# Kernel tuning notes

Measured on AMD Instinct MI355X. Metric: run time of the kernel, lower is better.

Reference implementation:

```python
import jax, jax.numpy as jnp
import numpy as np

EPS = 1e-5  # PyTorch BatchNorm2d default eps


def _batchnorm(x, gamma, beta):
    # training-mode BN over (N, T, V) per channel; x: [N, C, T, V]
    mean = jnp.mean(x, axis=(0, 2, 3), keepdims=True)
    var = jnp.var(x, axis=(0, 2, 3), keepdims=True)
    inv = jax.lax.rsqrt(var + EPS)
    return (x - mean) * inv * gamma[None, :, None, None] + beta[None, :, None, None]


def setup_inputs() -> dict:
    key = jax.random.key(0)
    ks = jax.random.split(key, 8)
    N, Cin, Cout, T, V, S = 64, 64, 128, 300, 25, 3
    x = jax.random.normal(ks[0], (N, Cin, T, V), dtype=jnp.float32)
    A = jax.random.uniform(ks[1], (S, V, V), dtype=jnp.float32)
    # per-subset 1x1 conv weights/biases (kaiming-ish scale)
    W = jax.random.normal(ks[2], (S, Cout, Cin), dtype=jnp.float32) / np.sqrt(Cin)
    b = jax.random.normal(ks[3], (S, Cout), dtype=jnp.float32) * 0.01
    alpha = jnp.zeros((1,), dtype=jnp.float32)
    bn_gamma = jnp.ones((Cout,), dtype=jnp.float32)
    bn_beta = jnp.zeros((Cout,), dtype=jnp.float32)
    # residual down path (in_channels != out_channels): conv1x1 + BN
    down_W = jax.random.normal(ks[4], (Cout, Cin), dtype=jnp.float32) / np.sqrt(Cin)
    down_b = jax.random.normal(ks[5], (Cout,), dtype=jnp.float32) * 0.01
    down_gamma = jnp.ones((Cout,), dtype=jnp.float32)
    down_beta = jnp.zeros((Cout,), dtype=jnp.float32)
    return {
        "x": x, "A": A, "W": W, "b": b, "alpha": alpha,
        "bn_gamma": bn_gamma, "bn_beta": bn_beta,
        "down_W": down_W, "down_b": down_b,
        "down_gamma": down_gamma, "down_beta": down_beta,
    }


def reference(x, A, W, b, alpha, bn_gamma, bn_beta, down_W, down_b, down_gamma, down_beta):
    V = x.shape[-1]
    eye = jnp.eye(V, dtype=x.dtype)
    A_adj = A + alpha[0] * eye[None]  # [S, V, V]
    # sum_s conv1x1_s( x @ A_s ): fuse adjacency matmul, 1x1 conv, subset sum
    y_agg = jnp.einsum('nctv,svw,soc->notw', x, A_adj, W)
    y_agg = y_agg + jnp.sum(b, axis=0)[None, :, None, None]
    y = _batchnorm(y_agg, bn_gamma, bn_beta)
    # residual down: 1x1 conv + BN (in_channels != out_channels)
    res = jnp.einsum('nctv,oc->notv', x, down_W) + down_b[None, :, None, None]
    res = _batchnorm(res, down_gamma, down_beta)
    return jax.nn.relu(y + res)
```

## Files before the change

kernel.cpp:

```cpp
#include <hip/hip_runtime.h>
#include <hip/hip_bf16.h>

#define N_   64
#define CIN  64
#define COUT 128
#define T_   300
#define V_   25
#define S_   3
#define NTV  (N_ * T_ * V_)

#define TS     10
#define NTB    (T_ / TS)
#define NBLK   (N_ * NTB)
#define RED_ROWS   64
#define RED_BLOCKS (NBLK / RED_ROWS)

#define WS_P    0
#define WS_P2   (WS_P + NBLK * 512)
#define WS_COEF (WS_P2 + RED_BLOCKS * 512)
#define WS_WF   (WS_COEF + 512)
#define WS_WSF  (WS_WF + 16384)
#define WS_AF   (WS_WSF + 16384)

typedef __attribute__((ext_vector_type(8))) short short8;
typedef __attribute__((ext_vector_type(4))) float f32x4;

#define LDS_BARRIER() asm volatile("s_waitcnt lgkmcnt(0)\n\ts_barrier" ::: "memory")

__device__ __forceinline__ unsigned short bfbits(float f) {
    union { __hip_bfloat16 h; unsigned short u; } cv;
    cv.h = __float2bfloat16(f);
    return cv.u;
}
__device__ __forceinline__ unsigned int pack2(float lo, float hi) {
    return (unsigned int)bfbits(lo) | ((unsigned int)bfbits(hi) << 16);
}

__device__ __forceinline__ int zoff(int nl, int k) {
    int slot = (k >> 3) ^ (nl & 31);
    return nl * 512 + slot * 16 + (k & 7) * 2;
}

__global__ __launch_bounds__(256) void k_prep(const float* __restrict__ W,
                                              const float* __restrict__ dW,
                                              const float* __restrict__ A,
                                              const float* __restrict__ alpha,
                                              unsigned short* __restrict__ Wf,
                                              unsigned short* __restrict__ Af) {
    int i = blockIdx.x * 256 + threadIdx.x;
    {
        int j = i & 7, lane = (i >> 3) & 63, ks = (i >> 9) & 7;
        int oh2 = i >> 12;
        int o = oh2 * 16 + (lane & 15);
        int k = ks * 32 + (lane >> 4) * 8 + j;
        float wv = (k < 192) ? W[(k >> 6) * (COUT * CIN) + o * CIN + (k & 63)]
                             : dW[o * CIN + (k - 192)];
        Wf[i] = bfbits(wv);
    }
    if (i < 4096) {
        int j = i & 7, lane = (i >> 3) & 63, wf = (i >> 9) & 1, s = i >> 10;
        int v = (lane >> 4) * 8 + j, w = wf * 16 + (lane & 15);
        float av;
        if (s < 3)
            av = (v < V_ && w < V_)
                   ? A[(s * V_ + v) * V_ + w] + ((v == w) ? alpha[0] : 0.f)
                   : 0.f;
        else
            av = (v == w && v < V_) ? 1.f : 0.f;
        Af[i] = bfbits(av);
    }
}

__global__ __launch_bounds__(256) void k_prep2(const float* __restrict__ W,
                                               const float* __restrict__ dW,
                                               const float* __restrict__ coef,
                                               unsigned short* __restrict__ Wsf) {
    int i = blockIdx.x * 256 + threadIdx.x;
    int j = i & 7, lane = (i >> 3) & 63, ks = (i >> 9) & 7;
    int oh2 = i >> 12;
    int o = oh2 * 16 + (lane & 15);
    int k = ks * 32 + (lane >> 4) * 8 + j;
    float wv = (k < 192) ? W[(k >> 6) * (COUT * CIN) + o * CIN + (k & 63)]
                         : dW[o * CIN + (k - 192)];
    float sc = (k < 192) ? coef[o] : coef[COUT + o];
    Wsf[i] = bfbits(wv * sc);
}

struct XRaw { f32x4 a0, a1; float s; };

__device__ __forceinline__ XRaw load_raw(const float* __restrict__ base, int lq) {
    XRaw r;
    if (lq < 3) {
        r.a0 = *(const f32x4*)(base + lq * 8);
        r.a1 = *(const f32x4*)(base + lq * 8 + 4);
        r.s = 0.f;
    } else {
        r.s = base[24];
        r.a0 = (f32x4){0.f, 0.f, 0.f, 0.f};
        r.a1 = (f32x4){0.f, 0.f, 0.f, 0.f};
    }
    return r;
}

__device__ __forceinline__ short8 cvt_xfr(const XRaw& x, int lq) {
    short8 r;
    if (lq < 3) {
#pragma unroll
        for (int j = 0; j < 4; ++j) {
            r[j]     = (short)bfbits(x.a0[j]);
            r[4 + j] = (short)bfbits(x.a1[j]);
        }
    } else {
        r[0] = (short)bfbits(x.s);
#pragma unroll
        for (int j = 1; j < 8; ++j) r[j] = 0;
    }
    return r;
}

__device__ __forceinline__ void stage(char* zb, const unsigned short* Alds,
                                      short8 xfr, int sp, int cq,
                                      int lq, int lr, int lane) {
    const f32x4 zero = {0.f, 0.f, 0.f, 0.f};
#pragma unroll
    for (int i = 0; i < 2; ++i) {
        const int s = 2 * sp + i;
#pragma unroll
        for (int wf = 0; wf < 2; ++wf) {
            short8 af = *(const short8*)(Alds + ((s * 2 + wf) * 64 + lane) * 8);
            f32x4 d = __builtin_amdgcn_mfma_f32_16x16x32_bf16(xfr, af, zero, 0, 0, 0);
            unsigned long long pk = (unsigned long long)pack2(d[0], d[1])
                                  | ((unsigned long long)pack2(d[2], d[3]) << 32);
            int row = wf * 16 + lr;
            int k = s * 64 + cq * 16 + lq * 4;
            *(unsigned long long*)(zb + zoff(row, k)) = pk;
        }
    }
}

template<bool STATS>
__global__ __launch_bounds__(512, 4) void k_gemm(
    const float* __restrict__ x, const unsigned short* __restrict__ Wf,
    const unsigned short* __restrict__ Af, const float* __restrict__ coef,
    float* __restrict__ P, float* __restrict__ out)
{
    __shared__ __align__(16) unsigned short Zt[2][32 * 256];
    __shared__ __align__(16) unsigned short Alds[8 * 64 * 8];

    const int tid = threadIdx.x;
    const int wid = tid >> 6, lane = tid & 63;
    const int lq = lane >> 4, lr = lane & 15;
    const int oh2 = wid;
    const int cq = wid & 3;
    const int sp = wid >> 2;

    const int bid = blockIdx.x;
    const int n = bid / NTB, tb = bid % NTB;
    const int t0 = tb * TS;

    if (tid < 512)
        *(short8*)(Alds + tid * 8) = *(const short8*)(Af + tid * 8);

    short8 wfr[8];
#pragma unroll
    for (int ks = 0; ks < 8; ++ks)
        wfr[ks] = *(const short8*)(Wf + (((oh2 * 8 + ks) * 64 + lane)) * 8);

    float c0v = 0.f;
    if (!STATS) c0v = coef[2 * COUT + oh2 * 16 + lr];

    float sy = 0.f, sy2 = 0.f, sr = 0.f, sr2 = 0.f;

    const int c = cq * 16 + lr;
    const float* xrow = x + ((size_t)(n * CIN + c) * T_) * V_;

    LDS_BARRIER();

    {
        XRaw r0 = load_raw(xrow + (size_t)t0 * V_, lq);
        stage((char*)Zt[0], Alds, cvt_xfr(r0, lq), sp, cq, lq, lr, lane);
    }
    XRaw slotA = load_raw(xrow + (size_t)(t0 + 1) * V_, lq);

    const f32x4 zero = {0.f, 0.f, 0.f, 0.f};

    for (int tt = 0; tt < TS; ++tt) {
        const int t = t0 + tt;
        char* zb = (char*)Zt[tt & 1];
        LDS_BARRIER();

        XRaw slotB;
        if (tt + 2 < TS) slotB = load_raw(xrow + (size_t)(t + 2) * V_, lq);
        else { slotB.a0 = zero; slotB.a1 = zero; slotB.s = 0.f; }

        if (tt + 1 < TS)
            stage((char*)Zt[(tt + 1) & 1], Alds, cvt_xfr(slotA, lq), sp, cq, lq, lr, lane);

        f32x4 acc[2], accr[2];
#pragma unroll
        for (int ks = 0; ks < 8; ++ks) {
            short8 za[2];
            za[0] = *(const short8*)(zb + zoff(lr, ks * 32 + lq * 8));
            za[1] = *(const short8*)(zb + zoff(16 + lr, ks * 32 + lq * 8));
            if constexpr (STATS) {
                if (ks < 6) {
#pragma unroll
                    for (int mf = 0; mf < 2; ++mf)
                        acc[mf] = __builtin_amdgcn_mfma_f32_16x16x32_bf16(
                            za[mf], wfr[ks], ks == 0 ? zero : acc[mf], 0, 0, 0);
                } else {
#pragma unroll
                    for (int mf = 0; mf < 2; ++mf)
                        accr[mf] = __builtin_amdgcn_mfma_f32_16x16x32_bf16(
                            za[mf], wfr[ks], ks == 6 ? zero : accr[mf], 0, 0, 0);
                }
            } else {
#pragma unroll
                for (int mf = 0; mf < 2; ++mf)
                    acc[mf] = __builtin_amdgcn_mfma_f32_16x16x32_bf16(
                        za[mf], wfr[ks], ks == 0 ? zero : acc[mf], 0, 0, 0);
            }
        }

        if constexpr (STATS) {
#pragma unroll
            for (int mf = 0; mf < 2; ++mf)
#pragma unroll
                for (int r = 0; r < 4; ++r) {
                    float yv = acc[mf][r];
                    sy += yv; sy2 = fmaf(yv, yv, sy2);
                    float rv = accr[mf][r];
                    sr += rv; sr2 = fmaf(rv, rv, sr2);
                }
        } else {
            const int o = oh2 * 16 + lr;
            float* rowp = out + ((size_t)(n * COUT + o) * T_ + t) * V_;
            f32x4 v0;
#pragma unroll
            for (int r = 0; r < 4; ++r) v0[r] = fmaxf(acc[0][r] + c0v, 0.f);
            *(f32x4*)(rowp + lq * 4) = v0;
            if (lq < 2) {
                f32x4 v1;
#pragma unroll
                for (int r = 0; r < 4; ++r) v1[r] = fmaxf(acc[1][r] + c0v, 0.f);
                *(f32x4*)(rowp + 16 + lq * 4) = v1;
            } else if (lq == 2) {
                rowp[24] = fmaxf(acc[1][0] + c0v, 0.f);
            }
        }

        slotA.a0 = slotB.a0; slotA.a1 = slotB.a1; slotA.s = slotB.s;
    }

    if constexpr (STATS) {
        sy  += __shfl_xor(sy, 16);  sy  += __shfl_xor(sy, 32);
        sy2 += __shfl_xor(sy2, 16); sy2 += __shfl_xor(sy2, 32);
        sr  += __shfl_xor(sr, 16);  sr  += __shfl_xor(sr, 32);
        sr2 += __shfl_xor(sr2, 16); sr2 += __shfl_xor(sr2, 32);
        if (lq == 0) {
            float* p = P + (size_t)bid * 512;
            const int o = oh2 * 16 + lr;
            p[o] = sy; p[128 + o] = sy2;
            p[256 + o] = sr; p[384 + o] = sr2;
        }
    }
}

__global__ __launch_bounds__(256) void k_red(const float* __restrict__ P,
                                             float* __restrict__ P2) {
    const int tid = threadIdx.x;
    float a0 = 0.f, a1 = 0.f;
    const int row0 = blockIdx.x * RED_ROWS;
    for (int r = 0; r < RED_ROWS; ++r) {
        const float* p = P + (size_t)(row0 + r) * 512;
        a0 += p[tid];
        a1 += p[256 + tid];
    }
    P2[blockIdx.x * 512 + tid] = a0;
    P2[blockIdx.x * 512 + 256 + tid] = a1;
}

__global__ __launch_bounds__(128) void k_coef(
    const float* __restrict__ P2, const float* __restrict__ gamma,
    const float* __restrict__ beta, const float* __restrict__ dgamma,
    const float* __restrict__ dbeta, const float* __restrict__ b,
    const float* __restrict__ db, float* __restrict__ coef) {
    const int o = threadIdx.x;
    float sy = 0.f, sy2 = 0.f, sr = 0.f, sr2 = 0.f;
    for (int r2 = 0; r2 < RED_BLOCKS; ++r2) {
        const float* p = P2 + r2 * 512;
        sy += p[o]; sy2 += p[128 + o]; sr += p[256 + o]; sr2 += p[384 + o];
    }
    const float bsum = b[o] + b[COUT + o] + b[2 * COUT + o];
    const float dbo = db[o];
    float syb  = sy + (float)NTV * bsum;
    float sy2b = sy2 + 2.f * bsum * sy + (float)NTV * bsum * bsum;
    float srb  = sr + (float)NTV * dbo;
    float sr2b = sr2 + 2.f * dbo * sr + (float)NTV * dbo * dbo;
    const float invn = 1.f / (float)NTV;
    float my = syb * invn, mr = srb * invn;
    float vy = fmaf(-my, my, sy2b * invn);
    float vr = fmaf(-mr, mr, sr2b * invn);
    float ay = rsqrtf(vy + 1e-5f) * gamma[o];
    float ar = rsqrtf(vr + 1e-5f) * dgamma[o];
    float c0 = beta[o] - my * ay + dbeta[o] - mr * ar + ay * bsum + ar * dbo;
    coef[o] = ay; coef[COUT + o] = ar; coef[2 * COUT + o] = c0;
}

extern "C" void kernel_launch(void* const* d_in, const int* in_sizes, int n_in,
                              void* d_out, int out_size, void* d_ws, size_t ws_size,
                              hipStream_t stream) {
    const float* x      = (const float*)d_in[0];
    const float* A      = (const float*)d_in[1];
    const float* W      = (const float*)d_in[2];
    const float* b      = (const float*)d_in[3];
    const float* alpha  = (const float*)d_in[4];
    const float* gamma  = (const float*)d_in[5];
    const float* beta   = (const float*)d_in[6];
    const float* dW     = (const float*)d_in[7];
    const float* db     = (const float*)d_in[8];
    const float* dgamma = (const float*)d_in[9];
    const float* dbeta  = (const float*)d_in[10];

    float* ws   = (float*)d_ws;
    float* P    = ws + WS_P;
    float* P2   = ws + WS_P2;
    float* coef = ws + WS_COEF;
    unsigned short* Wf  = (unsigned short*)(ws + WS_WF);
    unsigned short* Wsf = (unsigned short*)(ws + WS_WSF);
    unsigned short* Af  = (unsigned short*)(ws + WS_AF);
    float* out  = (float*)d_out;

    k_prep<<<128, 256, 0, stream>>>(W, dW, A, alpha, Wf, Af);
    k_gemm<true><<<NBLK, 512, 0, stream>>>(x, Wf, Af, nullptr, P, nullptr);
    k_red<<<RED_BLOCKS, 256, 0, stream>>>(P, P2);
    k_coef<<<1, 128, 0, stream>>>(P2, gamma, beta, dgamma, dbeta, b, db, coef);
    k_prep2<<<128, 256, 0, stream>>>(W, dW, coef, Wsf);
    k_gemm<false><<<NBLK, 512, 0, stream>>>(x, Wsf, Af, coef, nullptr, out);
}
```

Measured before the change: 224.6 us.

## Split each GEMM tile across two 256-thread blocks by output-channel half

Each former 512-thread block becomes two 256-thread blocks, each computing half of the output channels for the same (n, t-range) tile. Because of this, each block has to stage the full adjacency-multiplied Z tile by itself, so every wave now runs all 4 subset stages instead of 2. The aim is to give the scheduler more, smaller blocks and better occupancy. The cost is redundant staging MFMAs and x loads. The stats buffer is indexed per tile, and each half writes a disjoint set of channels.

Measured after the change: 242.9 us. +8.2%, slower.

```diff
diff --git a/kernel.cpp b/kernel.cpp
--- a/kernel.cpp
+++ b/kernel.cpp
@@ -11,12 +11,13 @@
 
 #define TS     10
 #define NTB    (T_ / TS)
-#define NBLK   (N_ * NTB)
+#define NTILE  (N_ * NTB)
+#define NBLK   (NTILE * 2)
 #define RED_ROWS   64
-#define RED_BLOCKS (NBLK / RED_ROWS)
+#define RED_BLOCKS (NTILE / RED_ROWS)
 
 #define WS_P    0
-#define WS_P2   (WS_P + NBLK * 512)
+#define WS_P2   (WS_P + NTILE * 512)
 #define WS_COEF (WS_P2 + RED_BLOCKS * 512)
 #define WS_WF   (WS_COEF + 512)
 #define WS_WSF  (WS_WF + 16384)
@@ -119,12 +120,11 @@
 }
 
 __device__ __forceinline__ void stage(char* zb, const unsigned short* Alds,
-                                      short8 xfr, int sp, int cq,
+                                      short8 xfr, int cq,
                                       int lq, int lr, int lane) {
     const f32x4 zero = {0.f, 0.f, 0.f, 0.f};
 #pragma unroll
-    for (int i = 0; i < 2; ++i) {
-        const int s = 2 * sp + i;
+    for (int s = 0; s < 4; ++s) {
 #pragma unroll
         for (int wf = 0; wf < 2; ++wf) {
             short8 af = *(const short8*)(Alds + ((s * 2 + wf) * 64 + lane) * 8);
@@ -139,7 +139,7 @@
 }
 
 template<bool STATS>
-__global__ __launch_bounds__(512, 4) void k_gemm(
+__global__ __launch_bounds__(256, 4) void k_gemm(
     const float* __restrict__ x, const unsigned short* __restrict__ Wf,
     const unsigned short* __restrict__ Af, const float* __restrict__ coef,
     float* __restrict__ P, float* __restrict__ out)
@@ -150,16 +150,17 @@
     const int tid = threadIdx.x;
     const int wid = tid >> 6, lane = tid & 63;
     const int lq = lane >> 4, lr = lane & 15;
-    const int oh2 = wid;
-    const int cq = wid & 3;
-    const int sp = wid >> 2;
 
     const int bid = blockIdx.x;
-    const int n = bid / NTB, tb = bid % NTB;
+    const int tile = bid >> 1, half = bid & 1;
+    const int n = tile / NTB, tb = tile % NTB;
     const int t0 = tb * TS;
 
-    if (tid < 512)
-        *(short8*)(Alds + tid * 8) = *(const short8*)(Af + tid * 8);
+    const int oh2 = half * 4 + wid;
+    const int cq = wid;
+
+    for (int i = tid; i < 512; i += 256)
+        *(short8*)(Alds + i * 8) = *(const short8*)(Af + i * 8);
 
     short8 wfr[8];
 #pragma unroll
@@ -178,7 +179,7 @@
 
     {
         XRaw r0 = load_raw(xrow + (size_t)t0 * V_, lq);
-        stage((char*)Zt[0], Alds, cvt_xfr(r0, lq), sp, cq, lq, lr, lane);
+        stage((char*)Zt[0], Alds, cvt_xfr(r0, lq), cq, lq, lr, lane);
     }
     XRaw slotA = load_raw(xrow + (size_t)(t0 + 1) * V_, lq);
 
@@ -194,7 +195,7 @@
         else { slotB.a0 = zero; slotB.a1 = zero; slotB.s = 0.f; }
 
         if (tt + 1 < TS)
-            stage((char*)Zt[(tt + 1) & 1], Alds, cvt_xfr(slotA, lq), sp, cq, lq, lr, lane);
+            stage((char*)Zt[(tt + 1) & 1], Alds, cvt_xfr(slotA, lq), cq, lq, lr, lane);
 
         f32x4 acc[2], accr[2];
 #pragma unroll
@@ -258,7 +259,7 @@
         sr  += __shfl_xor(sr, 16);  sr  += __shfl_xor(sr, 32);
         sr2 += __shfl_xor(sr2, 16); sr2 += __shfl_xor(sr2, 32);
         if (lq == 0) {
-            float* p = P + (size_t)bid * 512;
+            float* p = P + (size_t)tile * 512;
             const int o = oh2 * 16 + lr;
             p[o] = sy; p[128 + o] = sy2;
             p[256 + o] = sr; p[384 + o] = sr2;
@@ -332,9 +333,9 @@
     float* out  = (float*)d_out;
 
     k_prep<<<128, 256, 0, stream>>>(W, dW, A, alpha, Wf, Af);
-    k_gemm<true><<<NBLK, 512, 0, stream>>>(x, Wf, Af, nullptr, P, nullptr);
+    k_gemm<true><<<NBLK, 256, 0, stream>>>(x, Wf, Af, nullptr, P, nullptr);
     k_red<<<RED_BLOCKS, 256, 0, stream>>>(P, P2);
     k_coef<<<1, 128, 0, stream>>>(P2, gamma, beta, dgamma, dbeta, b, db, coef);
     k_prep2<<<128, 256, 0, stream>>>(W, dW, coef, Wsf);
-    k_gemm<false><<<NBLK, 512, 0, stream>>>(x, Wsf, Af, coef, nullptr, out);
-}
+    k_gemm<false><<<NBLK, 256, 0, stream>>>(x, Wsf, Af, coef, nullptr, out);
+}
```
